# Kernel tuning notes

Hardware: AMD Instinct MI355X
Metric: run time of the kernel (lower is better)

The kernel has to match this reference:

```python
import jax, jax.numpy as jnp
import numpy as np

N, E, D, L, G = 50000, 640000, 128, 5, 128
BN_EPS = 1e-5

def _bn(x, g, b):
    # training-mode batchnorm over axis 0, biased variance (torch semantics)
    m = x.mean(axis=0)
    v = x.var(axis=0)
    return (x - m) * jax.lax.rsqrt(v + BN_EPS) * g + b

def setup_inputs():
    key = jax.random.key(0)
    ks = iter(jax.random.split(key, 40))
    rn = lambda shape, s=0.05: jax.random.normal(next(ks), shape, jnp.float32) * s
    inp = {}
    inp['x'] = jax.random.randint(next(ks), (N, 1), 0, 300)
    inp['edge_index'] = jax.random.randint(next(ks), (2, E), 0, N)
    inp['edge_attr'] = jax.random.normal(next(ks), (E, 7), jnp.float32)
    inp['batch'] = jnp.sort(jax.random.randint(next(ks), (N,), 0, G))
    inp['node_emb'] = rn((300, D))
    inp['vn_emb'] = jnp.zeros((1, D), jnp.float32)
    inp['eps'] = jnp.zeros((L,), jnp.float32)
    inp['edge_W'] = rn((L, 7, D)); inp['edge_b'] = rn((L, D))
    inp['W1'] = rn((L, D, 2 * D)); inp['b1'] = rn((L, 2 * D))
    inp['bn1_g'] = 1.0 + rn((L, 2 * D)); inp['bn1_b'] = rn((L, 2 * D))
    inp['W2'] = rn((L, 2 * D, D)); inp['b2'] = rn((L, D))
    inp['bn_g'] = 1.0 + rn((L, D)); inp['bn_b'] = rn((L, D))
    inp['vn_W1'] = rn((L - 1, D, 2 * D)); inp['vn_b1'] = rn((L - 1, 2 * D))
    inp['vn_bn1_g'] = 1.0 + rn((L - 1, 2 * D)); inp['vn_bn1_b'] = rn((L - 1, 2 * D))
    inp['vn_W2'] = rn((L - 1, 2 * D, D)); inp['vn_b2'] = rn((L - 1, D))
    inp['vn_bn2_g'] = 1.0 + rn((L - 1, D)); inp['vn_bn2_b'] = rn((L - 1, D))
    return inp

def reference(x, edge_index, edge_attr, batch, node_emb, vn_emb, eps,
              edge_W, edge_b, W1, b1, bn1_g, bn1_b, W2, b2, bn_g, bn_b,
              vn_W1, vn_b1, vn_bn1_g, vn_bn1_b, vn_W2, vn_b2, vn_bn2_g, vn_bn2_b):
    src, dst = edge_index[0], edge_index[1]
    h = node_emb[x[:, 0]]                      # [N, D]
    vn = jnp.broadcast_to(vn_emb, (G, D))      # virtualnode state per graph
    for l in range(L):
        h_in = h + vn[batch]                   # virtualnode broadcast
        e = edge_attr @ edge_W[l] + edge_b[l]  # [E, D]
        msg = jax.nn.relu(h_in[src] + e)       # gather + fused elementwise
        agg = jax.ops.segment_sum(msg, dst, num_segments=N)
        z = (1.0 + eps[l]) * h_in + agg
        z = jax.nn.relu(_bn(z @ W1[l] + b1[l], bn1_g[l], bn1_b[l]))
        z = _bn(z @ W2[l] + b2[l], bn_g[l], bn_b[l])
        h_out = jax.nn.relu(z) if l != L - 1 else z
        if l < L - 1:
            pooled = jax.ops.segment_sum(h_in, batch, num_segments=G)
            v = vn + pooled
            v = jax.nn.relu(_bn(v @ vn_W1[l] + vn_b1[l], vn_bn1_g[l], vn_bn1_b[l]))
            vn = jax.nn.relu(_bn(v @ vn_W2[l] + vn_b2[l], vn_bn2_g[l], vn_bn2_b[l]))
        h = h_out
    return h
```

## Files before the change

kernel.cpp:

```cpp
#include <hip/hip_runtime.h>
#include <stdint.h>

#define NN 50000
#define EE 640000
#define DD 128
#define LL 5
#define GG 128
#define D2 256
#define CSRP_MAX 790016

using bf16x8 = __attribute__((ext_vector_type(8))) short;
using f32x4v = __attribute__((ext_vector_type(4))) float;
using u32x4v = __attribute__((ext_vector_type(4))) unsigned int;

__device__ __forceinline__ unsigned short f2bf(float f){
  union { float f; uint32_t u; } c; c.f = f;
  uint32_t u = c.u;
  uint32_t r = (u + 0x7FFFu + ((u >> 16) & 1u)) >> 16;
  return (unsigned short)r;
}
__device__ __forceinline__ float bf2f(unsigned short u){
  union { uint32_t u; float f; } c; c.u = ((uint32_t)u) << 16; return c.f;
}
__device__ __forceinline__ float bf2f_lo(uint32_t p){
  union { uint32_t u; float f; } c; c.u = p << 16; return c.f;
}
__device__ __forceinline__ float bf2f_hi(uint32_t p){
  union { uint32_t u; float f; } c; c.u = p & 0xFFFF0000u; return c.f;
}


__global__ __launch_bounds__(256) void zero_kernel(float* p, int n){
  int i = blockIdx.x*256 + threadIdx.x;
  if (i < n) p[i] = 0.f;
}

__global__ __launch_bounds__(256) void count_kernel(const int* __restrict__ ei, int* __restrict__ counts){
  int e = blockIdx.x*256 + threadIdx.x;
  if (e < EE) atomicAdd(&counts[ei[EE + e]], 1);
}

#define SCAN_B 512
__global__ __launch_bounds__(SCAN_B) void scan1_kernel(const int* __restrict__ counts, int* __restrict__ bsums, int n){
  __shared__ int sh[SCAN_B];
  int b = blockIdx.x, t = threadIdx.x;
  int i = b*SCAN_B + t;
  sh[t] = (i < n) ? ((counts[i] + 3) & ~3) : 0;
  __syncthreads();
  for (int s = SCAN_B/2; s > 0; s >>= 1){
    if (t < s) sh[t] += sh[t+s];
    __syncthreads();
  }
  if (t == 0) bsums[b] = sh[0];
}

__global__ void scan2_kernel(int* bsums, int nb){
  if (threadIdx.x == 0){
    int run = 0;
    for (int i = 0; i < nb; ++i){ int v = bsums[i]; bsums[i] = run; run += v; }
  }
}

__global__ __launch_bounds__(SCAN_B) void scan3_kernel(const int* __restrict__ counts, const int* __restrict__ bsums,
                                                       int* __restrict__ startp, int* __restrict__ cursor, int n){
  __shared__ int sh[SCAN_B];
  int b = blockIdx.x, t = threadIdx.x;
  int i = b*SCAN_B + t;
  int v = (i < n) ? ((counts[i] + 3) & ~3) : 0;
  sh[t] = v;
  __syncthreads();
  for (int s = 1; s < SCAN_B; s <<= 1){
    int add = (t >= s) ? sh[t-s] : 0;
    __syncthreads();
    sh[t] += add;
    __syncthreads();
  }
  int excl = sh[t] - v + bsums[b];
  if (i < n){ startp[i] = excl; cursor[i] = excl; }
  if (i == n-1) startp[n] = excl + v;
}

__global__ __launch_bounds__(256) void csrinit_kernel(int* __restrict__ csr_src, unsigned short* __restrict__ csr_eah){
  int i = blockIdx.x*256 + threadIdx.x;
  if (i < CSRP_MAX){
    csr_src[i] = NN;
    u32x4v z = {0,0,0,0};
    *(u32x4v*)(csr_eah + (size_t)i*8) = z;
  }
}

__global__ __launch_bounds__(256) void fillcvt_kernel(const int* __restrict__ ei, const float* __restrict__ ea,
                                                      int* __restrict__ cursor,
                                                      int* __restrict__ csr_src, unsigned short* __restrict__ csr_eah){
  int e = blockIdx.x*256 + threadIdx.x;
  if (e < EE){
    int d = ei[EE + e];
    int slot = atomicAdd(&cursor[d], 1);
    csr_src[slot] = ei[e];
    unsigned short t[8];
    #pragma unroll
    for (int k = 0; k < 7; ++k) t[k] = f2bf(ea[(size_t)e*7 + k]);
    t[7] = 0;
    u32x4v pv;
    pv[0] = (uint32_t)t[0] | ((uint32_t)t[1] << 16);
    pv[1] = (uint32_t)t[2] | ((uint32_t)t[3] << 16);
    pv[2] = (uint32_t)t[4] | ((uint32_t)t[5] << 16);
    pv[3] = (uint32_t)t[6] | ((uint32_t)t[7] << 16);
    *(u32x4v*)(csr_eah + (size_t)slot*8) = pv;
  }
}

__global__ __launch_bounds__(256) void wtrans_kernel(const float* __restrict__ W1, const float* __restrict__ W2,
                                                     unsigned short* __restrict__ W1T, unsigned short* __restrict__ W2T){
  int idx = blockIdx.x*256 + threadIdx.x;
  const int total = LL*DD*D2;
  if (idx < total){
    int l = idx / (DD*D2);
    int rem = idx - l*(DD*D2);
    int k = rem / D2;
    int c = rem - k*D2;
    W1T[(size_t)l*32768 + (size_t)c*128 + k] = f2bf(W1[idx]);
  } else if (idx < 2*total){
    int j = idx - total;
    int l = j / (DD*D2);
    int rem = j - l*(DD*D2);
    int k = rem / DD;
    int c = rem - k*DD;
    W2T[(size_t)l*32768 + (size_t)c*256 + k] = f2bf(W2[j]);
  }
}

__global__ __launch_bounds__(128) void init_kernel(const int* __restrict__ x, const int* __restrict__ batch,
                                                   const float* __restrict__ emb, const float* __restrict__ vn_emb,
                                                   unsigned short* __restrict__ hin_bf, float* __restrict__ vbuf0,
                                                   float* __restrict__ vn){
  int r0 = blockIdx.x*128;
  int r1 = r0 + 128; if (r1 > NN) r1 = NN;
  int d = threadIdx.x;
  float ve = vn_emb[d];
  if (blockIdx.x == 0){
    for (int g = 0; g < GG; ++g) vn[(size_t)g*DD + d] = ve;
    hin_bf[(size_t)NN*DD + d] = 0xFF80u;
  }
  __shared__ int sb[128];
  __shared__ int sx[128];
  if (r0 + d < r1){ sb[d] = batch[r0 + d]; sx[d] = x[r0 + d]; }
  __syncthreads();
  int curg = sb[0];
  float pacc = 0.f;
  for (int r = r0; r < r1; ++r){
    int g = sb[r - r0];
    if (g != curg){
      atomicAdd(&vbuf0[(size_t)curg*DD + d], pacc);
      pacc = 0.f; curg = g;
    }
    float hv = emb[(size_t)sx[r - r0]*DD + d] + ve;
    hin_bf[(size_t)r*DD + d] = f2bf(hv);
    pacc += hv;
  }
  atomicAdd(&vbuf0[(size_t)curg*DD + d], pacc);
}


__global__ __launch_bounds__(256) void agg4_kernel(const unsigned short* __restrict__ hin_bf,
                                                   const int* __restrict__ csr_src,
                                                   const unsigned short* __restrict__ csr_eah,
                                                   const int* __restrict__ startp,
                                                   const float* __restrict__ eW, const float* __restrict__ eb,
                                                   const float* __restrict__ eps, int l,
                                                   unsigned short* __restrict__ zout){
  const int wid  = threadIdx.x >> 6;
  const int lane = threadIdx.x & 63;
  const int node = blockIdx.x*4 + wid;
  const int s0 = startp[node], s1 = startp[node+1];
  float2 w[7];
  #pragma unroll
  for (int k = 0; k < 7; ++k) w[k] = *(const float2*)(eW + k*128 + lane*2);
  const float2 bd = *(const float2*)(eb + lane*2);
  float acc0 = 0.f, acc1 = 0.f;
  for (int s = s0; s < s1; s += 4){
    const int4 sv = *(const int4*)(csr_src + s);
    u32x4v p0 = *(const u32x4v*)(csr_eah + (size_t)s*8);
    u32x4v p1 = *(const u32x4v*)(csr_eah + (size_t)s*8 + 8);
    u32x4v p2 = *(const u32x4v*)(csr_eah + (size_t)s*8 + 16);
    u32x4v p3 = *(const u32x4v*)(csr_eah + (size_t)s*8 + 24);
    uint32_t h0 = *(const uint32_t*)(hin_bf + (size_t)sv.x*128 + lane*2);
    uint32_t h1 = *(const uint32_t*)(hin_bf + (size_t)sv.y*128 + lane*2);
    uint32_t h2 = *(const uint32_t*)(hin_bf + (size_t)sv.z*128 + lane*2);
    uint32_t h3 = *(const uint32_t*)(hin_bf + (size_t)sv.w*128 + lane*2);
#define EDGE(P, H) { \
    float a0v = bf2f_lo(P[0]), a1v = bf2f_hi(P[0]); \
    float a2v = bf2f_lo(P[1]), a3v = bf2f_hi(P[1]); \
    float a4v = bf2f_lo(P[2]), a5v = bf2f_hi(P[2]); \
    float a6v = bf2f_lo(P[3]); \
    float e0 = bd.x + a0v*w[0].x + a1v*w[1].x + a2v*w[2].x + a3v*w[3].x + a4v*w[4].x + a5v*w[5].x + a6v*w[6].x; \
    float e1 = bd.y + a0v*w[0].y + a1v*w[1].y + a2v*w[2].y + a3v*w[3].y + a4v*w[4].y + a5v*w[5].y + a6v*w[6].y; \
    float m0 = bf2f_lo(H) + e0, m1 = bf2f_hi(H) + e1; \
    acc0 += (m0 > 0.f) ? m0 : 0.f; \
    acc1 += (m1 > 0.f) ? m1 : 0.f; }
    EDGE(p0, h0)
    EDGE(p1, h1)
    EDGE(p2, h2)
    EDGE(p3, h3)
#undef EDGE
  }
  const float one = 1.f + eps[l];
  uint32_t hs = *(const uint32_t*)(hin_bf + (size_t)node*128 + lane*2);
  float z0 = one*bf2f_lo(hs) + acc0;
  float z1 = one*bf2f_hi(hs) + acc1;
  uint32_t out = (uint32_t)f2bf(z0) | ((uint32_t)f2bf(z1) << 16);
  *(uint32_t*)(zout + (size_t)node*128 + lane*2) = out;
}

__global__ __launch_bounds__(256) void gemm1_kernel(const unsigned short* __restrict__ A,
                                                    const unsigned short* __restrict__ BT,
                                                    const float* __restrict__ bias,
                                                    unsigned short* __restrict__ Y,
                                                    float* __restrict__ sums, float* __restrict__ sqs){
  __shared__ __align__(16) unsigned short Al[128*128];
  __shared__ __align__(16) unsigned short Bl[128*128];
  const int t = threadIdx.x;
  const int rb = blockIdx.x, cb = blockIdx.y;
  for (int it = 0; it < 8; ++it){
    int idx = it*256 + t;
    int row = idx >> 4, ch = idx & 15;
    int grow = rb*128 + row;
    u32x4v v = {0,0,0,0};
    if (grow < NN) v = *(const u32x4v*)(A + (size_t)grow*128 + ch*8);
    *(u32x4v*)((char*)Al + row*256 + ((ch*16) ^ ((row&7)<<4))) = v;
  }
  for (int it = 0; it < 8; ++it){
    int idx = it*256 + t;
    int row = idx >> 4, ch = idx & 15;
    u32x4v v = *(const u32x4v*)(BT + (size_t)(cb*128 + row)*128 + ch*8);
    *(u32x4v*)((char*)Bl + row*256 + ((ch*16) ^ ((row&7)<<4))) = v;
  }
  __syncthreads();
  const int lane = t & 63, wave = t >> 6;
  const int wm = wave >> 1, wn = wave & 1;
  const int r0 = lane & 15, kg = lane >> 4;
  f32x4v acc[4][4] = {};
  #pragma unroll
  for (int kk = 0; kk < 4; ++kk){
    const int kb = kk*64 + kg*16;
    bf16x8 a[4], b[4];
    #pragma unroll
    for (int m = 0; m < 4; ++m){
      int row = wm*64 + m*16 + r0;
      a[m] = *(const bf16x8*)((const char*)Al + row*256 + (kb ^ ((r0&7)<<4)));
    }
    #pragma unroll
    for (int n = 0; n < 4; ++n){
      int col = wn*64 + n*16 + r0;
      b[n] = *(const bf16x8*)((const char*)Bl + col*256 + (kb ^ ((r0&7)<<4)));
    }
    #pragma unroll
    for (int m = 0; m < 4; ++m)
      #pragma unroll
      for (int n = 0; n < 4; ++n)
        acc[m][n] = __builtin_amdgcn_mfma_f32_16x16x32_bf16(a[m], b[n], acc[m][n], 0, 0, 0);
  }
  #pragma unroll
  for (int n = 0; n < 4; ++n){
    const int col = cb*128 + wn*64 + n*16 + r0;
    const float bv = bias[col];
    float s = 0.f, q = 0.f;
    #pragma unroll
    for (int m = 0; m < 4; ++m){
      const int rowb = rb*128 + wm*64 + m*16 + kg*4;
      #pragma unroll
      for (int j = 0; j < 4; ++j){
        int grow = rowb + j;
        if (grow < NN){
          float v = acc[m][n][j] + bv;
          Y[(size_t)grow*256 + col] = f2bf(v);
          s += v; q += v*v;
        }
      }
    }
    s += __shfl_xor(s, 16); q += __shfl_xor(q, 16);
    s += __shfl_xor(s, 32); q += __shfl_xor(q, 32);
    if (kg == 0){ atomicAdd(&sums[col], s); atomicAdd(&sqs[col], q); }
  }
}

template<int FINAL>
__global__ __launch_bounds__(256) void gemm2_kernel(const unsigned short* __restrict__ Yin,
                                                    const float* __restrict__ sum1, const float* __restrict__ sq1,
                                                    const float* __restrict__ bg, const float* __restrict__ bb,
                                                    const unsigned short* __restrict__ BT,
                                                    const float* __restrict__ bias,
                                                    unsigned short* __restrict__ Yh, float* __restrict__ Yf,
                                                    float* __restrict__ sums, float* __restrict__ sqs){
  __shared__ __align__(16) unsigned short Al[128*128];
  __shared__ __align__(16) unsigned short Bl[128*128];
  __shared__ float s_scl[256], s_shf[256];
  const int t = threadIdx.x;
  const int rb = blockIdx.x;
  {
    const float invn = 1.f/(float)NN;
    float m = sum1[t]*invn;
    float var = sq1[t]*invn - m*m;
    var = var > 0.f ? var : 0.f;
    float sc = bg[t]*rsqrtf(var + 1e-5f);
    s_scl[t] = sc;
    s_shf[t] = bb[t] - m*sc;
  }
  const int lane = t & 63, wave = t >> 6;
  const int wm = wave >> 1, wn = wave & 1;
  const int r0 = lane & 15, kg = lane >> 4;
  f32x4v acc[4][4] = {};
  for (int kt = 0; kt < 2; ++kt){
    __syncthreads();
    for (int it = 0; it < 8; ++it){
      int idx = it*256 + t;
      int row = idx >> 4, ch = idx & 15;
      int grow = rb*128 + row;
      int c0 = kt*128 + ch*8;
      u32x4v pv = {0,0,0,0};
      if (grow < NN){
        u32x4v yv = *(const u32x4v*)(Yin + (size_t)grow*256 + c0);
        unsigned short tb[8];
        #pragma unroll
        for (int jj = 0; jj < 4; ++jj){
          uint32_t pw = yv[jj];
          float a0 = bf2f((unsigned short)(pw & 0xFFFFu));
          float a1 = bf2f((unsigned short)(pw >> 16));
          float v0 = a0*s_scl[c0 + 2*jj]     + s_shf[c0 + 2*jj];
          float v1 = a1*s_scl[c0 + 2*jj + 1] + s_shf[c0 + 2*jj + 1];
          tb[2*jj]     = f2bf(v0 > 0.f ? v0 : 0.f);
          tb[2*jj + 1] = f2bf(v1 > 0.f ? v1 : 0.f);
        }
        pv[0] = (uint32_t)tb[0] | ((uint32_t)tb[1] << 16);
        pv[1] = (uint32_t)tb[2] | ((uint32_t)tb[3] << 16);
        pv[2] = (uint32_t)tb[4] | ((uint32_t)tb[5] << 16);
        pv[3] = (uint32_t)tb[6] | ((uint32_t)tb[7] << 16);
      }
      *(u32x4v*)((char*)Al + row*256 + ((ch*16) ^ ((row&7)<<4))) = pv;
    }
    for (int it = 0; it < 8; ++it){
      int idx = it*256 + t;
      int row = idx >> 4, ch = idx & 15;
      u32x4v v = *(const u32x4v*)(BT + (size_t)row*256 + kt*128 + ch*8);
      *(u32x4v*)((char*)Bl + row*256 + ((ch*16) ^ ((row&7)<<4))) = v;
    }
    __syncthreads();
    #pragma unroll
    for (int kk = 0; kk < 4; ++kk){
      const int kb = kk*64 + kg*16;
      bf16x8 a[4], b[4];
      #pragma unroll
      for (int m = 0; m < 4; ++m){
        int row = wm*64 + m*16 + r0;
        a[m] = *(const bf16x8*)((const char*)Al + row*256 + (kb ^ ((r0&7)<<4)));
      }
      #pragma unroll
      for (int n = 0; n < 4; ++n){
        int col = wn*64 + n*16 + r0;
        b[n] = *(const bf16x8*)((const char*)Bl + col*256 + (kb ^ ((r0&7)<<4)));
      }
      #pragma unroll
      for (int m = 0; m < 4; ++m)
        #pragma unroll
        for (int n = 0; n < 4; ++n)
          acc[m][n] = __builtin_amdgcn_mfma_f32_16x16x32_bf16(a[m], b[n], acc[m][n], 0, 0, 0);
    }
  }
  #pragma unroll
  for (int n = 0; n < 4; ++n){
    const int col = wn*64 + n*16 + r0;
    const float bv = bias[col];
    float s = 0.f, q = 0.f;
    #pragma unroll
    for (int m = 0; m < 4; ++m){
      const int rowb = rb*128 + wm*64 + m*16 + kg*4;
      #pragma unroll
      for (int j = 0; j < 4; ++j){
        int grow = rowb + j;
        if (grow < NN){
          float v = acc[m][n][j] + bv;
          if (FINAL) Yf[(size_t)grow*128 + col] = v;
          else       Yh[(size_t)grow*128 + col] = f2bf(v);
          s += v; q += v*v;
        }
      }
    }
    s += __shfl_xor(s, 16); q += __shfl_xor(q, 16);
    s += __shfl_xor(s, 32); q += __shfl_xor(q, 32);
    if (kg == 0){ atomicAdd(&sums[col], s); atomicAdd(&sqs[col], q); }
  }
}

__global__ __launch_bounds__(128) void happly_fused_kernel(const unsigned short* __restrict__ y2h,
                                                           const float* __restrict__ sum2, const float* __restrict__ sq2,
                                                           const float* __restrict__ bg, const float* __restrict__ bb,
                                                           const float* __restrict__ vn, const int* __restrict__ batch,
                                                           unsigned short* __restrict__ hin_bf, float* __restrict__ vbuf_next){
  int r0 = blockIdx.x*128;
  int r1 = r0 + 128; if (r1 > NN) r1 = NN;
  int d = threadIdx.x;
  const float invn = 1.f/(float)NN;
  float m = sum2[d]*invn;
  float var = sq2[d]*invn - m*m;
  var = var > 0.f ? var : 0.f;
  float sc = bg[d]*rsqrtf(var + 1e-5f);
  float sh = bb[d] - m*sc;
  __shared__ int sb[128];
  if (r0 + d < r1) sb[d] = batch[r0 + d];
  __syncthreads();
  int curg = sb[0];
  float vnv = vn[(size_t)curg*DD + d];
  float pacc = 0.f;
  for (int r = r0; r < r1; ++r){
    int g = sb[r - r0];
    if (g != curg){
      atomicAdd(&vbuf_next[(size_t)curg*DD + d], pacc);
      pacc = 0.f; curg = g;
      vnv = vn[(size_t)curg*DD + d];
    }
    float y = bf2f(y2h[(size_t)r*DD + d]);
    float v = y*sc + sh;
    v = v > 0.f ? v : 0.f;
    float hv = v + vnv;
    hin_bf[(size_t)r*DD + d] = f2bf(hv);
    pacc += hv;
  }
  atomicAdd(&vbuf_next[(size_t)curg*DD + d], pacc);
}

__global__ __launch_bounds__(256) void happly_final_kernel(float* __restrict__ y,
                                                           const float* __restrict__ sum2, const float* __restrict__ sq2,
                                                           const float* __restrict__ bg, const float* __restrict__ bb){
  int idx = blockIdx.x*256 + threadIdx.x;
  if (idx >= NN*32) return;
  int c4 = idx & 31;
  const float invn = 1.f/(float)NN;
  f32x4v yv = *(const f32x4v*)(y + (size_t)idx*4);
  f32x4v o;
  #pragma unroll
  for (int j = 0; j < 4; ++j){
    int c = c4*4 + j;
    float m = sum2[c]*invn;
    float var = sq2[c]*invn - m*m;
    var = var > 0.f ? var : 0.f;
    float sc = bg[c]*rsqrtf(var + 1e-5f);
    o[j] = (yv[j] - m)*sc + bb[c];
  }
  *(f32x4v*)(y + (size_t)idx*4) = o;
}

__global__ __launch_bounds__(256) void vmlp1_kernel(const float* __restrict__ vn, const float* __restrict__ vbufl,
                                                    const float* __restrict__ W, const float* __restrict__ bias,
                                                    float* __restrict__ Yo,
                                                    float* __restrict__ sums, float* __restrict__ sqs){
  __shared__ float vrow[128];
  int r = blockIdx.x, c = threadIdx.x;
  if (c < 128) vrow[c] = vn[r*128 + c] + vbufl[r*128 + c];
  __syncthreads();
  float acc = 0.f;
  #pragma unroll 8
  for (int k = 0; k < 128; ++k) acc += vrow[k]*W[k*256 + c];
  float y = acc + bias[c];
  Yo[r*256 + c] = y;
  atomicAdd(&sums[c], y);
  atomicAdd(&sqs[c], y*y);
}

__global__ __launch_bounds__(128) void vmlp2_kernel(const float* __restrict__ Yin,
                                                    const float* __restrict__ sumv1, const float* __restrict__ sqv1,
                                                    const float* __restrict__ vg, const float* __restrict__ vb,
                                                    const float* __restrict__ W, const float* __restrict__ bias,
                                                    float* __restrict__ Yo,
                                                    float* __restrict__ sums, float* __restrict__ sqs){
  __shared__ float arow[256];
  __shared__ float s_scl[256], s_shf[256];
  int r = blockIdx.x, c = threadIdx.x;
  const float invg = 1.f/(float)GG;
  for (int k = c; k < 256; k += 128){
    float m = sumv1[k]*invg;
    float var = sqv1[k]*invg - m*m;
    var = var > 0.f ? var : 0.f;
    float sc = vg[k]*rsqrtf(var + 1e-5f);
    s_scl[k] = sc;
    s_shf[k] = vb[k] - m*sc;
  }
  __syncthreads();
  for (int k = c; k < 256; k += 128){
    float a = Yin[r*256 + k]*s_scl[k] + s_shf[k];
    arow[k] = a > 0.f ? a : 0.f;
  }
  __syncthreads();
  float acc = 0.f;
  #pragma unroll 8
  for (int k = 0; k < 256; ++k) acc += arow[k]*W[k*128 + c];
  float y = acc + bias[c];
  Yo[r*128 + c] = y;
  atomicAdd(&sums[c], y);
  atomicAdd(&sqs[c], y*y);
}

__global__ __launch_bounds__(256) void va_kernel(const float* __restrict__ yv2,
                                                 const float* __restrict__ sumv2, const float* __restrict__ sqv2,
                                                 const float* __restrict__ vg, const float* __restrict__ vb,
                                                 float* __restrict__ vn){
  int idx = blockIdx.x*256 + threadIdx.x;
  if (idx < GG*128){
    int c = idx & 127;
    const float invg = 1.f/(float)GG;
    float m = sumv2[c]*invg;
    float var = sqv2[c]*invg - m*m;
    var = var > 0.f ? var : 0.f;
    float sc = vg[c]*rsqrtf(var + 1e-5f);
    float v = (yv2[idx] - m)*sc + vb[c];
    vn[idx] = v > 0.f ? v : 0.f;
  }
}


extern "C" void kernel_launch(void* const* d_in, const int* in_sizes, int n_in,
                              void* d_out, int out_size, void* d_ws, size_t ws_size,
                              hipStream_t stream){
  const int*   x         = (const int*)  d_in[0];
  const int*   ei        = (const int*)  d_in[1];
  const float* edge_attr = (const float*)d_in[2];
  const int*   batch     = (const int*)  d_in[3];
  const float* node_emb  = (const float*)d_in[4];
  const float* vn_emb    = (const float*)d_in[5];
  const float* eps       = (const float*)d_in[6];
  const float* edge_W    = (const float*)d_in[7];
  const float* edge_b    = (const float*)d_in[8];
  const float* W1        = (const float*)d_in[9];
  const float* b1        = (const float*)d_in[10];
  const float* bn1_g     = (const float*)d_in[11];
  const float* bn1_b     = (const float*)d_in[12];
  const float* W2        = (const float*)d_in[13];
  const float* b2        = (const float*)d_in[14];
  const float* bn_g      = (const float*)d_in[15];
  const float* bn_b      = (const float*)d_in[16];
  const float* vn_W1     = (const float*)d_in[17];
  const float* vn_b1     = (const float*)d_in[18];
  const float* vn_bn1_g  = (const float*)d_in[19];
  const float* vn_bn1_b  = (const float*)d_in[20];
  const float* vn_W2     = (const float*)d_in[21];
  const float* vn_b2     = (const float*)d_in[22];
  const float* vn_bn2_g  = (const float*)d_in[23];
  const float* vn_bn2_b  = (const float*)d_in[24];
  float* hout = (float*)d_out;

  char* ws = (char*)d_ws;
  size_t off = 0;
  auto alloc = [&](size_t bytes)->char*{
    char* p = ws + off; off += (bytes + 255) & ~(size_t)255; return p;
  };
  unsigned short* hin_bf = (unsigned short*)alloc((size_t)(NN+1)*DD*2);
  unsigned short* zy     = (unsigned short*)alloc((size_t)NN*DD*2);
  unsigned short* y1h    = (unsigned short*)alloc((size_t)NN*D2*2);
  float*          vn     = (float*)         alloc((size_t)GG*DD*4);
  float*          yv1    = (float*)         alloc((size_t)GG*D2*4);
  float*          yv2    = (float*)         alloc((size_t)GG*DD*4);
  unsigned short* W1T    = (unsigned short*)alloc((size_t)LL*D2*DD*2);
  unsigned short* W2T    = (unsigned short*)alloc((size_t)LL*D2*DD*2);
  const int STATS_F = LL*8*256;
  const int VBUF_F  = 5*GG*DD;
  const int ZTOT    = STATS_F + VBUF_F + NN;
  float* zeroreg = (float*)alloc((size_t)ZTOT*4);
  float* stats_all = zeroreg;
  float* vbuf_all  = zeroreg + STATS_F;
  int*   counts    = (int*)(zeroreg + STATS_F + VBUF_F);
  int*   startp = (int*)  alloc((size_t)(NN+1)*4);
  int*   cursor = (int*)  alloc((size_t)NN*4);
  int*   bsums  = (int*)  alloc(128*4);
  int*   csr_src= (int*)  alloc((size_t)CSRP_MAX*4);
  unsigned short* csr_eah = (unsigned short*)alloc((size_t)CSRP_MAX*8*2);

  const int nb_scan = (NN + SCAN_B - 1)/SCAN_B;
  const int row_blocks = (NN + 127)/128;
  const int ew_blocks = (NN*32 + 255)/256;

  zero_kernel<<<(ZTOT + 255)/256, 256, 0, stream>>>(zeroreg, ZTOT);
  csrinit_kernel<<<(CSRP_MAX + 255)/256, 256, 0, stream>>>(csr_src, csr_eah);
  count_kernel<<<EE/256, 256, 0, stream>>>(ei, counts);
  scan1_kernel<<<nb_scan, SCAN_B, 0, stream>>>(counts, bsums, NN);
  scan2_kernel<<<1, 64, 0, stream>>>(bsums, nb_scan);
  scan3_kernel<<<nb_scan, SCAN_B, 0, stream>>>(counts, bsums, startp, cursor, NN);
  fillcvt_kernel<<<EE/256, 256, 0, stream>>>(ei, edge_attr, cursor, csr_src, csr_eah);
  wtrans_kernel<<<(2*LL*DD*D2 + 255)/256, 256, 0, stream>>>(W1, W2, W1T, W2T);
  init_kernel<<<row_blocks, 128, 0, stream>>>(x, batch, node_emb, vn_emb, hin_bf, vbuf_all, vn);

  for (int l = 0; l < LL; ++l){
    float* st    = stats_all + (size_t)l*8*256;
    float* sum1  = st + 0*256, *sq1  = st + 1*256;
    float* sum2  = st + 2*256, *sq2  = st + 3*256;
    float* sumv1 = st + 4*256, *sqv1 = st + 5*256;
    float* sumv2 = st + 6*256, *sqv2 = st + 7*256;

    agg4_kernel<<<NN/4, 256, 0, stream>>>(hin_bf, csr_src, csr_eah, startp,
                                          edge_W + (size_t)l*7*DD, edge_b + (size_t)l*DD, eps, l, zy);
    gemm1_kernel<<<dim3(row_blocks, 2), 256, 0, stream>>>(zy, W1T + (size_t)l*32768,
                                                          b1 + (size_t)l*D2, y1h, sum1, sq1);
    if (l != LL-1){
      gemm2_kernel<0><<<row_blocks, 256, 0, stream>>>(y1h, sum1, sq1,
                                                      bn1_g + (size_t)l*D2, bn1_b + (size_t)l*D2,
                                                      W2T + (size_t)l*32768, b2 + (size_t)l*DD,
                                                      zy, nullptr, sum2, sq2);
      float* vbufl = vbuf_all + (size_t)l*GG*DD;
      float* vbufn = vbuf_all + (size_t)(l+1)*GG*DD;
      vmlp1_kernel<<<GG, 256, 0, stream>>>(vn, vbufl, vn_W1 + (size_t)l*DD*D2, vn_b1 + (size_t)l*D2,
                                           yv1, sumv1, sqv1);
      vmlp2_kernel<<<GG, 128, 0, stream>>>(yv1, sumv1, sqv1,
                                           vn_bn1_g + (size_t)l*D2, vn_bn1_b + (size_t)l*D2,
                                           vn_W2 + (size_t)l*D2*DD, vn_b2 + (size_t)l*DD,
                                           yv2, sumv2, sqv2);
      va_kernel<<<(GG*DD + 255)/256, 256, 0, stream>>>(yv2, sumv2, sqv2,
                                                       vn_bn2_g + (size_t)l*DD, vn_bn2_b + (size_t)l*DD, vn);
      happly_fused_kernel<<<row_blocks, 128, 0, stream>>>(zy, sum2, sq2,
                                                          bn_g + (size_t)l*DD, bn_b + (size_t)l*DD,
                                                          vn, batch, hin_bf, vbufn);
    } else {
      gemm2_kernel<1><<<row_blocks, 256, 0, stream>>>(y1h, sum1, sq1,
                                                      bn1_g + (size_t)l*D2, bn1_b + (size_t)l*D2,
                                                      W2T + (size_t)l*32768, b2 + (size_t)l*DD,
                                                      nullptr, hout, sum2, sq2);
      happly_final_kernel<<<ew_blocks, 256, 0, stream>>>(hout, sum2, sq2,
                                                         bn_g + (size_t)l*DD, bn_b + (size_t)l*DD);
    }
  }
  (void)in_sizes; (void)n_in; (void)out_size; (void)ws_size;
}
```

Measured before the change: 1.263 ms.

## Load GEMM operands directly from global memory and shrink happly row blocks

gemm1 now skips LDS staging entirely and reads its A and B fragments straight from global memory. gemm2 does the same for the weight matrix B while still staging the BN-transformed activations in LDS. This is meant to cut LDS use and barriers, which should allow more resident blocks, at the cost of uncoalesced or repeated global and L2 reads. The zy and y1h buffers are padded so the unguarded tail rows can be read safely. happly_fused now processes 32 rows per block instead of 128, launching more blocks for better parallelism.

```diff
diff --git a/kernel.cpp b/kernel.cpp
--- a/kernel.cpp
+++ b/kernel.cpp
@@ -8,6 +8,7 @@
 #define GG 128
 #define D2 256
 #define CSRP_MAX 790016
+#define HROWS 32
 
 using bf16x8 = __attribute__((ext_vector_type(8))) short;
 using f32x4v = __attribute__((ext_vector_type(4))) float;
@@ -217,28 +218,13 @@
                                                     const float* __restrict__ bias,
                                                     unsigned short* __restrict__ Y,
                                                     float* __restrict__ sums, float* __restrict__ sqs){
-  __shared__ __align__(16) unsigned short Al[128*128];
-  __shared__ __align__(16) unsigned short Bl[128*128];
   const int t = threadIdx.x;
   const int rb = blockIdx.x, cb = blockIdx.y;
-  for (int it = 0; it < 8; ++it){
-    int idx = it*256 + t;
-    int row = idx >> 4, ch = idx & 15;
-    int grow = rb*128 + row;
-    u32x4v v = {0,0,0,0};
-    if (grow < NN) v = *(const u32x4v*)(A + (size_t)grow*128 + ch*8);
-    *(u32x4v*)((char*)Al + row*256 + ((ch*16) ^ ((row&7)<<4))) = v;
-  }
-  for (int it = 0; it < 8; ++it){
-    int idx = it*256 + t;
-    int row = idx >> 4, ch = idx & 15;
-    u32x4v v = *(const u32x4v*)(BT + (size_t)(cb*128 + row)*128 + ch*8);
-    *(u32x4v*)((char*)Bl + row*256 + ((ch*16) ^ ((row&7)<<4))) = v;
-  }
-  __syncthreads();
   const int lane = t & 63, wave = t >> 6;
   const int wm = wave >> 1, wn = wave & 1;
   const int r0 = lane & 15, kg = lane >> 4;
+  const char* Ab = (const char*)A;
+  const char* Bb = (const char*)BT;
   f32x4v acc[4][4] = {};
   #pragma unroll
   for (int kk = 0; kk < 4; ++kk){
@@ -246,13 +232,13 @@
     bf16x8 a[4], b[4];
     #pragma unroll
     for (int m = 0; m < 4; ++m){
-      int row = wm*64 + m*16 + r0;
-      a[m] = *(const bf16x8*)((const char*)Al + row*256 + (kb ^ ((r0&7)<<4)));
+      int row = rb*128 + wm*64 + m*16 + r0;
+      a[m] = *(const bf16x8*)(Ab + (size_t)row*256 + kb);
     }
     #pragma unroll
     for (int n = 0; n < 4; ++n){
-      int col = wn*64 + n*16 + r0;
-      b[n] = *(const bf16x8*)((const char*)Bl + col*256 + (kb ^ ((r0&7)<<4)));
+      int colg = cb*128 + wn*64 + n*16 + r0;
+      b[n] = *(const bf16x8*)(Bb + (size_t)colg*256 + kb);
     }
     #pragma unroll
     for (int m = 0; m < 4; ++m)
@@ -293,7 +279,6 @@
                                                     unsigned short* __restrict__ Yh, float* __restrict__ Yf,
                                                     float* __restrict__ sums, float* __restrict__ sqs){
   __shared__ __align__(16) unsigned short Al[128*128];
-  __shared__ __align__(16) unsigned short Bl[128*128];
   __shared__ float s_scl[256], s_shf[256];
   const int t = threadIdx.x;
   const int rb = blockIdx.x;
@@ -309,6 +294,7 @@
   const int lane = t & 63, wave = t >> 6;
   const int wm = wave >> 1, wn = wave & 1;
   const int r0 = lane & 15, kg = lane >> 4;
+  const char* Bb = (const char*)BT;
   f32x4v acc[4][4] = {};
   for (int kt = 0; kt < 2; ++kt){
     __syncthreads();
@@ -338,12 +324,6 @@
       }
       *(u32x4v*)((char*)Al + row*256 + ((ch*16) ^ ((row&7)<<4))) = pv;
     }
-    for (int it = 0; it < 8; ++it){
-      int idx = it*256 + t;
-      int row = idx >> 4, ch = idx & 15;
-      u32x4v v = *(const u32x4v*)(BT + (size_t)row*256 + kt*128 + ch*8);
-      *(u32x4v*)((char*)Bl + row*256 + ((ch*16) ^ ((row&7)<<4))) = v;
-    }
     __syncthreads();
     #pragma unroll
     for (int kk = 0; kk < 4; ++kk){
@@ -356,8 +336,8 @@
       }
       #pragma unroll
       for (int n = 0; n < 4; ++n){
-        int col = wn*64 + n*16 + r0;
-        b[n] = *(const bf16x8*)((const char*)Bl + col*256 + (kb ^ ((r0&7)<<4)));
+        int colg = wn*64 + n*16 + r0;
+        b[n] = *(const bf16x8*)(Bb + (size_t)colg*512 + kt*256 + kb);
       }
       #pragma unroll
       for (int m = 0; m < 4; ++m)
@@ -396,8 +376,8 @@
                                                            const float* __restrict__ bg, const float* __restrict__ bb,
                                                            const float* __restrict__ vn, const int* __restrict__ batch,
                                                            unsigned short* __restrict__ hin_bf, float* __restrict__ vbuf_next){
-  int r0 = blockIdx.x*128;
-  int r1 = r0 + 128; if (r1 > NN) r1 = NN;
+  int r0 = blockIdx.x*HROWS;
+  int r1 = r0 + HROWS; if (r1 > NN) r1 = NN;
   int d = threadIdx.x;
   const float invn = 1.f/(float)NN;
   float m = sum2[d]*invn;
@@ -405,8 +385,8 @@
   var = var > 0.f ? var : 0.f;
   float sc = bg[d]*rsqrtf(var + 1e-5f);
   float sh = bb[d] - m*sc;
-  __shared__ int sb[128];
-  if (r0 + d < r1) sb[d] = batch[r0 + d];
+  __shared__ int sb[HROWS];
+  if (d < HROWS && r0 + d < r1) sb[d] = batch[r0 + d];
   __syncthreads();
   int curg = sb[0];
   float vnv = vn[(size_t)curg*DD + d];
@@ -553,8 +533,8 @@
     char* p = ws + off; off += (bytes + 255) & ~(size_t)255; return p;
   };
   unsigned short* hin_bf = (unsigned short*)alloc((size_t)(NN+1)*DD*2);
-  unsigned short* zy     = (unsigned short*)alloc((size_t)NN*DD*2);
-  unsigned short* y1h    = (unsigned short*)alloc((size_t)NN*D2*2);
+  unsigned short* zy     = (unsigned short*)alloc((size_t)(NN+64)*DD*2);
+  unsigned short* y1h    = (unsigned short*)alloc((size_t)(NN+64)*D2*2);
   float*          vn     = (float*)         alloc((size_t)GG*DD*4);
   float*          yv1    = (float*)         alloc((size_t)GG*D2*4);
   float*          yv2    = (float*)         alloc((size_t)GG*DD*4);
@@ -575,6 +555,7 @@
 
   const int nb_scan = (NN + SCAN_B - 1)/SCAN_B;
   const int row_blocks = (NN + 127)/128;
+  const int hap_blocks = (NN + HROWS - 1)/HROWS;
   const int ew_blocks = (NN*32 + 255)/256;
 
   zero_kernel<<<(ZTOT + 255)/256, 256, 0, stream>>>(zeroreg, ZTOT);
@@ -613,7 +594,7 @@
                                            yv2, sumv2, sqv2);
       va_kernel<<<(GG*DD + 255)/256, 256, 0, stream>>>(yv2, sumv2, sqv2,
                                                        vn_bn2_g + (size_t)l*DD, vn_bn2_b + (size_t)l*DD, vn);
-      happly_fused_kernel<<<row_blocks, 128, 0, stream>>>(zy, sum2, sq2,
+      happly_fused_kernel<<<hap_blocks, 128, 0, stream>>>(zy, sum2, sq2,
                                                           bn_g + (size_t)l*DD, bn_b + (size_t)l*DD,
                                                           vn, batch, hin_bf, vbufn);
     } else {
```

After: 1.187 ms. 6.0% less time.
